# Optimization experiments

Measured on AMD Instinct MI355X. Metric: run time of the kernel, lower is better.

The kernel has to match this reference:

```python
import jax, jax.numpy as jnp
import numpy as np

N_NODES = 50000
N_EDGES = 400000


def _gcn_norm(edge_index, num_nodes):
    """Add self-loops and compute symmetric GCN normalization coefficients.

    Returns (src, dst, norm) where out[dst] += norm * h[src].
    """
    loop = jnp.arange(num_nodes, dtype=edge_index.dtype)
    src = jnp.concatenate([edge_index[0], loop])
    dst = jnp.concatenate([edge_index[1], loop])
    ones = jnp.ones(src.shape[0], dtype=jnp.float32)
    deg = jax.ops.segment_sum(ones, dst, num_segments=num_nodes)
    d_inv_sqrt = jnp.where(deg > 0, jax.lax.rsqrt(jnp.maximum(deg, 1.0)), 0.0)
    norm = d_inv_sqrt[src] * d_inv_sqrt[dst]
    return src, dst, norm


def _gcn_conv(x, W, b, src, dst, norm, num_nodes):
    h = x @ W                              # [N, out] dense GEMM first (PyG GCNConv order)
    msg = h[src] * norm[:, None]           # [E+N, out] gather + scale
    agg = jax.ops.segment_sum(msg, dst, num_segments=num_nodes)  # scatter-add
    return agg + b


def setup_inputs() -> dict:
    key = jax.random.key(0)
    k1, k2, k3, k4, k5, k6 = jax.random.split(key, 6)
    x = jax.random.normal(k1, (N_NODES, 128), dtype=jnp.float32)
    edge_index = jax.random.randint(k2, (2, N_EDGES), 0, N_NODES, dtype=jnp.int64)
    # Glorot-ish scaled params
    W1 = jax.random.normal(k3, (128, 512), dtype=jnp.float32) * (1.0 / np.sqrt(128))
    b1 = jnp.zeros((512,), dtype=jnp.float32)
    W2 = jax.random.normal(k4, (512, 250), dtype=jnp.float32) * (1.0 / np.sqrt(512))
    b2 = jnp.zeros((250,), dtype=jnp.float32)
    return {"x": x, "edge_index": edge_index, "W1": W1, "b1": b1, "W2": W2, "b2": b2}


def reference(x, edge_index, W1, b1, W2, b2):
    num_nodes = x.shape[0]
    src, dst, norm = _gcn_norm(edge_index, num_nodes)
    h = _gcn_conv(x, W1, b1, src, dst, norm, num_nodes)
    h = jax.nn.relu(h)
    h = _gcn_conv(h, W2, b2, src, dst, norm, num_nodes)
    return jax.nn.relu(h)
```

## Files before the change

### kernel.cpp

```cpp
#include <hip/hip_runtime.h>

constexpr int NN  = 50000;
constexpr int NE  = 400000;
constexpr int F0  = 128;
constexpr int F1  = 512;
constexpr int F2  = 250;
constexpr int MT  = 391;
constexpr int SCAN_N = 50176;
constexpr int SCAN_B = 49;

typedef short  short8 __attribute__((ext_vector_type(8)));
typedef float  f32x4  __attribute__((ext_vector_type(4)));

__device__ inline unsigned short f2bf(float f) {
    union { float f; unsigned u; } v; v.f = f;
    unsigned u = v.u;
    return (unsigned short)((u + 0x7FFFu + ((u >> 16) & 1u)) >> 16);
}
__device__ inline float bf2f(unsigned short h) {
    union { unsigned u; float f; } v; v.u = ((unsigned)h) << 16;
    return v.f;
}

__global__ void k_hist(const int4* __restrict__ dst4, int* __restrict__ cnt) {
    int t = blockIdx.x * 256 + threadIdx.x;
    if (t >= NE / 4) return;
    int4 d = dst4[t];
    atomicAdd(&cnt[d.x], 1); atomicAdd(&cnt[d.y], 1);
    atomicAdd(&cnt[d.z], 1); atomicAdd(&cnt[d.w], 1);
}

__global__ __launch_bounds__(256) void k_scanA(const int4* __restrict__ cnt4,
                                               int* __restrict__ bsum) {
    __shared__ int lds[256];
    const int b = blockIdx.x, t = threadIdx.x;
    int4 c = cnt4[b * 256 + t];
    lds[t] = c.x + c.y + c.z + c.w;
    __syncthreads();
    for (int d = 128; d > 0; d >>= 1) {
        if (t < d) lds[t] += lds[t + d];
        __syncthreads();
    }
    if (t == 0) bsum[b] = lds[0];
}
__global__ void k_scanB(const int* __restrict__ bsum, int* __restrict__ boff) {
    int t = threadIdx.x;
    int v = (t < SCAN_B) ? bsum[t] : 0;
    int orig = v;
    for (int d = 1; d < 64; d <<= 1) {
        int u = __shfl_up(v, d);
        if (t >= d) v += u;
    }
    if (t < SCAN_B) boff[t] = v - orig;
}
__global__ __launch_bounds__(256) void k_scanC(const int4* __restrict__ cnt4,
                                               const int* __restrict__ boff,
                                               int* __restrict__ off,
                                               float* __restrict__ dinv) {
    __shared__ int lds[256];
    const int b = blockIdx.x, t = threadIdx.x;
    int4 c = cnt4[b * 256 + t];
    int s = c.x + c.y + c.z + c.w;
    lds[t] = s;
    __syncthreads();
    for (int d = 1; d < 256; d <<= 1) {
        int add = (t >= d) ? lds[t - d] : 0;
        __syncthreads();
        lds[t] += add;
        __syncthreads();
    }
    int run = boff[b] + lds[t] - s;
    int base = b * 1024 + t * 4;
    if (base < NN) { off[base] = run; dinv[base] = rsqrtf((float)c.x + 1.0f); }
    run += c.x;
    if (base + 1 < NN) { off[base + 1] = run; dinv[base + 1] = rsqrtf((float)c.y + 1.0f); }
    run += c.y;
    if (base + 2 < NN) { off[base + 2] = run; dinv[base + 2] = rsqrtf((float)c.z + 1.0f); }
    run += c.z;
    if (base + 3 < NN) { off[base + 3] = run; dinv[base + 3] = rsqrtf((float)c.w + 1.0f); }
    if (b == 0 && t == 0) off[NN] = NE;
}

__global__ void k_bucket(const int4* __restrict__ src4, const int4* __restrict__ dst4,
                         const int* __restrict__ off, int* __restrict__ cnt,
                         int* __restrict__ csr) {
    int t = blockIdx.x * 256 + threadIdx.x;
    if (t >= NE / 4) return;
    int4 s = src4[t];
    int4 d = dst4[t];
    csr[off[d.x] + atomicSub(&cnt[d.x], 1) - 1] = s.x;
    csr[off[d.y] + atomicSub(&cnt[d.y], 1) - 1] = s.y;
    csr[off[d.z] + atomicSub(&cnt[d.z], 1) - 1] = s.z;
    csr[off[d.w] + atomicSub(&cnt[d.w], 1) - 1] = s.w;
}

__global__ __launch_bounds__(256) void k_prep(
        const float4* __restrict__ x4, const float* __restrict__ dinv,
        ushort4* __restrict__ xs,
        const float* __restrict__ W1, unsigned short* __restrict__ w1t,
        const float* __restrict__ W2, unsigned short* __restrict__ w2t) {
    int b = blockIdx.x;
    if (b < 6250) {
        int t = b * 256 + threadIdx.x;
        float dn = dinv[t >> 5];
        float4 v = x4[t];
        ushort4 o;
        o.x = f2bf(dn * v.x); o.y = f2bf(dn * v.y);
        o.z = f2bf(dn * v.z); o.w = f2bf(dn * v.w);
        xs[t] = o;
    } else if (b < 6250 + 256) {
        int t = (b - 6250) * 256 + threadIdx.x;
        int n = t >> 7, k = t & 127;
        w1t[t] = f2bf(W1[k * F1 + n]);
    } else {
        int t = (b - 6506) * 256 + threadIdx.x;
        int n = t >> 9, k = t & 511;
        w2t[t] = (n < F2) ? f2bf(W2[k * F2 + n]) : (unsigned short)0;
    }
}

__global__ __launch_bounds__(256) void k_gather1(
        const ushort4* __restrict__ xs, const int* __restrict__ off,
        const int* __restrict__ csr, const float* __restrict__ dinv,
        ushort4* __restrict__ agg) {
    int n = blockIdx.x * 8 + (threadIdx.x >> 5);
    int c = threadIdx.x & 31;
    if (n >= NN) return;
    float dn = dinv[n];
    ushort4 a = xs[(size_t)n * 32 + c];
    float sx = bf2f(a.x), sy = bf2f(a.y), sz = bf2f(a.z), sw = bf2f(a.w);
    int j = off[n], e1 = off[n + 1];
    for (; j + 4 <= e1; j += 4) {
        int s0 = csr[j], s1 = csr[j + 1], s2 = csr[j + 2], s3 = csr[j + 3];
        ushort4 v0 = xs[(size_t)s0 * 32 + c];
        ushort4 v1 = xs[(size_t)s1 * 32 + c];
        ushort4 v2 = xs[(size_t)s2 * 32 + c];
        ushort4 v3 = xs[(size_t)s3 * 32 + c];
        sx += bf2f(v0.x) + bf2f(v1.x) + bf2f(v2.x) + bf2f(v3.x);
        sy += bf2f(v0.y) + bf2f(v1.y) + bf2f(v2.y) + bf2f(v3.y);
        sz += bf2f(v0.z) + bf2f(v1.z) + bf2f(v2.z) + bf2f(v3.z);
        sw += bf2f(v0.w) + bf2f(v1.w) + bf2f(v2.w) + bf2f(v3.w);
    }
    for (; j < e1; ++j) {
        int s = csr[j];
        ushort4 v = xs[(size_t)s * 32 + c];
        sx += bf2f(v.x); sy += bf2f(v.y); sz += bf2f(v.z); sw += bf2f(v.w);
    }
    ushort4 o;
    o.x = f2bf(dn * sx); o.y = f2bf(dn * sy); o.z = f2bf(dn * sz); o.w = f2bf(dn * sw);
    agg[(size_t)n * 32 + c] = o;
}

__global__ __launch_bounds__(256) void k_gather2(
        const ushort4* __restrict__ t4, const int* __restrict__ off,
        const int* __restrict__ csr, const float* __restrict__ dinv,
        const float* __restrict__ b2, float* __restrict__ out) {
    int n = blockIdx.x * 4 + (threadIdx.x >> 6);
    int c = threadIdx.x & 63;
    if (n >= NN) return;
    float dn = dinv[n];
    ushort4 a = t4[(size_t)n * 64 + c];
    float sx = bf2f(a.x), sy = bf2f(a.y), sz = bf2f(a.z), sw = bf2f(a.w);
    int j = off[n], e1 = off[n + 1];
    for (; j + 4 <= e1; j += 4) {
        int s0 = csr[j], s1 = csr[j + 1], s2 = csr[j + 2], s3 = csr[j + 3];
        ushort4 v0 = t4[(size_t)s0 * 64 + c];
        ushort4 v1 = t4[(size_t)s1 * 64 + c];
        ushort4 v2 = t4[(size_t)s2 * 64 + c];
        ushort4 v3 = t4[(size_t)s3 * 64 + c];
        sx += bf2f(v0.x) + bf2f(v1.x) + bf2f(v2.x) + bf2f(v3.x);
        sy += bf2f(v0.y) + bf2f(v1.y) + bf2f(v2.y) + bf2f(v3.y);
        sz += bf2f(v0.z) + bf2f(v1.z) + bf2f(v2.z) + bf2f(v3.z);
        sw += bf2f(v0.w) + bf2f(v1.w) + bf2f(v2.w) + bf2f(v3.w);
    }
    for (; j < e1; ++j) {
        int s = csr[j];
        ushort4 v = t4[(size_t)s * 64 + c];
        sx += bf2f(v.x); sy += bf2f(v.y); sz += bf2f(v.z); sw += bf2f(v.w);
    }
    int f = c * 4;
    float* o = out + (size_t)n * F2;
    if (f     < F2) o[f]     = fmaxf(dn * sx + b2[f],     0.f);
    if (f + 1 < F2) o[f + 1] = fmaxf(dn * sy + b2[f + 1], 0.f);
    if (f + 2 < F2) o[f + 2] = fmaxf(dn * sz + b2[f + 2], 0.f);
    if (f + 3 < F2) o[f + 3] = fmaxf(dn * sw + b2[f + 3], 0.f);
}

__global__ __launch_bounds__(256) void k_gemm_bf16(
        const unsigned short* __restrict__ A, int lda,
        const unsigned short* __restrict__ Bt, int ldb,
        unsigned short* __restrict__ C, int ldc,
        const float* __restrict__ bias, int do_relu,
        const float* __restrict__ rowscale,
        int M, int K)
{
    __shared__ unsigned short As[128 * 32];
    __shared__ unsigned short Bs[128 * 32];

    const int tid = threadIdx.x;
    const int wv = tid >> 6, ln = tid & 63;
    const int m0 = blockIdx.y * 128, n0 = blockIdx.x * 128;
    const int wy = wv >> 1, wx = wv & 1;
    const int lane15 = ln & 15, quad = ln >> 4;

    const unsigned short* ag[2];
    const unsigned short* bg[2];
    int ldsoff[2];
#pragma unroll
    for (int i = 0; i < 2; ++i) {
        int c = (i * 4 + wv) * 64 + ln;
        int m = c >> 2, q = c & 3;
        int gq = q ^ ((m >> 1) & 3);
        int arow = m0 + m; if (arow > M - 1) arow = M - 1;
        ag[i] = A  + (size_t)arow * lda + gq * 8;
        bg[i] = Bt + (size_t)(n0 + m) * ldb + gq * 8;
        ldsoff[i] = (i * 4 + wv) * 512;
    }

    f32x4 acc[4][4];
#pragma unroll
    for (int fy = 0; fy < 4; ++fy)
#pragma unroll
        for (int fx = 0; fx < 4; ++fx)
            acc[fy][fx] = (f32x4)0.0f;

    for (int k0 = 0; k0 < K; k0 += 32) {
#pragma unroll
        for (int i = 0; i < 2; ++i) {
            __builtin_amdgcn_global_load_lds(
                (const __attribute__((address_space(1))) void*)ag[i],
                (__attribute__((address_space(3))) void*)(As + ldsoff[i]), 16, 0, 0);
            __builtin_amdgcn_global_load_lds(
                (const __attribute__((address_space(1))) void*)bg[i],
                (__attribute__((address_space(3))) void*)(Bs + ldsoff[i]), 16, 0, 0);
            ag[i] += 32; bg[i] += 32;
        }
        __syncthreads();

        short8 af[4], bf[4];
#pragma unroll
        for (int f = 0; f < 4; ++f) {
            int mA = wy * 64 + f * 16 + lane15;
            int sA = quad ^ ((mA >> 1) & 3);
            af[f] = *(const short8*)(As + mA * 32 + sA * 8);
            int nB = wx * 64 + f * 16 + lane15;
            int sB = quad ^ ((nB >> 1) & 3);
            bf[f] = *(const short8*)(Bs + nB * 32 + sB * 8);
        }
#pragma unroll
        for (int fy = 0; fy < 4; ++fy)
#pragma unroll
            for (int fx = 0; fx < 4; ++fx)
                acc[fy][fx] = __builtin_amdgcn_mfma_f32_16x16x32_bf16(
                    af[fy], bf[fx], acc[fy][fx], 0, 0, 0);
        __syncthreads();
    }

#pragma unroll
    for (int fy = 0; fy < 4; ++fy) {
        int rowb = m0 + wy * 64 + fy * 16 + quad * 4;
        float rs[4] = {1.f, 1.f, 1.f, 1.f};
        if (rowscale) {
#pragma unroll
            for (int r = 0; r < 4; ++r) {
                int row = rowb + r; if (row > M - 1) row = M - 1;
                rs[r] = rowscale[row];
            }
        }
#pragma unroll
        for (int fx = 0; fx < 4; ++fx) {
            int col = n0 + wx * 64 + fx * 16 + lane15;
            float bia = bias ? bias[col] : 0.0f;
            f32x4 v = acc[fy][fx];
#pragma unroll
            for (int r = 0; r < 4; ++r) {
                int row = rowb + r;
                if (row < M) {
                    float val = v[r] + bia;
                    if (do_relu) val = fmaxf(val, 0.0f);
                    val *= rs[r];
                    C[(size_t)row * ldc + col] = f2bf(val);
                }
            }
        }
    }
}

extern "C" void kernel_launch(void* const* d_in, const int* in_sizes, int n_in,
                              void* d_out, int out_size, void* d_ws, size_t ws_size,
                              hipStream_t stream) {
    const float* x  = (const float*)d_in[0];
    const int*   ei = (const int*)d_in[1];
    const float* W1 = (const float*)d_in[2];
    const float* b1 = (const float*)d_in[3];
    const float* W2 = (const float*)d_in[4];
    const float* b2 = (const float*)d_in[5];
    float* out = (float*)d_out;

    char* p = (char*)d_ws;
    auto carve = [&](size_t bytes) { char* r = p; p += (bytes + 255) & ~(size_t)255; return r; };
    float*          dinv = (float*)carve(NN * 4);
    int*            cnt  = (int*)carve(SCAN_N * 4);
    int*            off  = (int*)carve((NN + 1) * 4);
    int*            csr  = (int*)carve(NE * 4);
    int*            bsum = (int*)carve(64 * 4);
    int*            boff = (int*)carve(64 * 4);
    unsigned short* xs   = (unsigned short*)carve((size_t)NN * F0 * 2);
    unsigned short* agg1 = (unsigned short*)carve((size_t)NN * F0 * 2);
    unsigned short* h1   = (unsigned short*)carve((size_t)NN * F1 * 2);
    unsigned short* t2s  = (unsigned short*)carve((size_t)NN * 256 * 2);
    unsigned short* w1t  = (unsigned short*)carve((size_t)F1 * F0 * 2);
    unsigned short* w2t  = (unsigned short*)carve((size_t)256 * F1 * 2);

    hipMemsetAsync(cnt, 0, SCAN_N * sizeof(int), stream);
    k_hist <<<(NE / 4 + 255) / 256, 256, 0, stream>>>((const int4*)(ei + NE), cnt);
    k_scanA<<<SCAN_B, 256, 0, stream>>>((const int4*)cnt, bsum);
    k_scanB<<<1, 64, 0, stream>>>(bsum, boff);
    k_scanC<<<SCAN_B, 256, 0, stream>>>((const int4*)cnt, boff, off, dinv);
    k_bucket<<<(NE / 4 + 255) / 256, 256, 0, stream>>>(
        (const int4*)ei, (const int4*)(ei + NE), off, cnt, csr);

    k_prep<<<6250 + 256 + 512, 256, 0, stream>>>(
        (const float4*)x, dinv, (ushort4*)xs, W1, w1t, W2, w2t);

    k_gather1<<<(NN + 7) / 8, 256, 0, stream>>>((const ushort4*)xs, off, csr, dinv,
                                                (ushort4*)agg1);
    k_gemm_bf16<<<dim3(F1 / 128, MT), 256, 0, stream>>>(
        agg1, F0, w1t, F0, h1, F1, b1, 1, nullptr, NN, F0);

    k_gemm_bf16<<<dim3(256 / 128, MT), 256, 0, stream>>>(
        h1, F1, w2t, F1, t2s, 256, nullptr, 0, dinv, NN, F1);
    k_gather2<<<(NN + 3) / 4, 256, 0, stream>>>((const ushort4*)t2s, off, csr, dinv,
                                                b2, out);
}
```

Before: 292.1 us.

## Double-buffer LDS in bf16 GEMM and shrink M tile to 64 rows

The GEMM kernel now uses 64x128 output tiles instead of 128x128, which doubles the number of blocks launched for both layers. It also double-buffers the A and B shared-memory tiles, issuing the next K-slice's global-to-LDS loads before computing on the current slice, so one barrier per iteration replaces two. The intent is to raise occupancy and wave count on the GPU and to overlap global loads with MFMA work. The cost is less reuse of each B tile per block and more LDS per block.

```diff
diff --git a/kernel.cpp b/kernel.cpp
--- a/kernel.cpp
+++ b/kernel.cpp
@@ -5,7 +5,7 @@
 constexpr int F0  = 128;
 constexpr int F1  = 512;
 constexpr int F2  = 250;
-constexpr int MT  = 391;
+constexpr int MT64 = 782;
 constexpr int SCAN_N = 50176;
 constexpr int SCAN_B = 49;
 
@@ -194,71 +194,91 @@
         const float* __restrict__ rowscale,
         int M, int K)
 {
-    __shared__ unsigned short As[128 * 32];
-    __shared__ unsigned short Bs[128 * 32];
+    __shared__ unsigned short As[2][64 * 32];
+    __shared__ unsigned short Bs[2][128 * 32];
 
     const int tid = threadIdx.x;
     const int wv = tid >> 6, ln = tid & 63;
-    const int m0 = blockIdx.y * 128, n0 = blockIdx.x * 128;
+    const int m0 = blockIdx.y * 64, n0 = blockIdx.x * 128;
     const int wy = wv >> 1, wx = wv & 1;
     const int lane15 = ln & 15, quad = ln >> 4;
 
-    const unsigned short* ag[2];
-    const unsigned short* bg[2];
-    int ldsoff[2];
+    {
+    }
+    const int cA = tid, mA_ = cA >> 2, qA = cA & 3;
+    const int gqA = qA ^ ((mA_ >> 1) & 3);
+    int arow = m0 + mA_; if (arow > M - 1) arow = M - 1;
+    const unsigned short* agp = A + (size_t)arow * lda + gqA * 8;
+    const int aofs = wv * 512;
+
+    const unsigned short* bgp[2];
+    int bofs[2];
 #pragma unroll
     for (int i = 0; i < 2; ++i) {
         int c = (i * 4 + wv) * 64 + ln;
         int m = c >> 2, q = c & 3;
         int gq = q ^ ((m >> 1) & 3);
-        int arow = m0 + m; if (arow > M - 1) arow = M - 1;
-        ag[i] = A  + (size_t)arow * lda + gq * 8;
-        bg[i] = Bt + (size_t)(n0 + m) * ldb + gq * 8;
-        ldsoff[i] = (i * 4 + wv) * 512;
-    }
-
-    f32x4 acc[4][4];
-#pragma unroll
-    for (int fy = 0; fy < 4; ++fy)
+        bgp[i] = Bt + (size_t)(n0 + m) * ldb + gq * 8;
+        bofs[i] = (i * 4 + wv) * 512;
+    }
+
+    f32x4 acc[2][4];
+#pragma unroll
+    for (int fy = 0; fy < 2; ++fy)
 #pragma unroll
         for (int fx = 0; fx < 4; ++fx)
             acc[fy][fx] = (f32x4)0.0f;
 
-    for (int k0 = 0; k0 < K; k0 += 32) {
-#pragma unroll
-        for (int i = 0; i < 2; ++i) {
+    const int NK = K >> 5;
+
+    __builtin_amdgcn_global_load_lds(
+        (const __attribute__((address_space(1))) void*)agp,
+        (__attribute__((address_space(3))) void*)(&As[0][0] + aofs), 16, 0, 0);
+#pragma unroll
+    for (int i = 0; i < 2; ++i)
+        __builtin_amdgcn_global_load_lds(
+            (const __attribute__((address_space(1))) void*)bgp[i],
+            (__attribute__((address_space(3))) void*)(&Bs[0][0] + bofs[i]), 16, 0, 0);
+
+    for (int ks = 0; ks < NK; ++ks) {
+        __syncthreads();
+        if (ks + 1 < NK) {
+            int ko = (ks + 1) << 5;
+            int nb = (ks + 1) & 1;
             __builtin_amdgcn_global_load_lds(
-                (const __attribute__((address_space(1))) void*)ag[i],
-                (__attribute__((address_space(3))) void*)(As + ldsoff[i]), 16, 0, 0);
-            __builtin_amdgcn_global_load_lds(
-                (const __attribute__((address_space(1))) void*)bg[i],
-                (__attribute__((address_space(3))) void*)(Bs + ldsoff[i]), 16, 0, 0);
-            ag[i] += 32; bg[i] += 32;
-        }
-        __syncthreads();
-
-        short8 af[4], bf[4];
+                (const __attribute__((address_space(1))) void*)(agp + ko),
+                (__attribute__((address_space(3))) void*)(&As[nb][0] + aofs), 16, 0, 0);
+#pragma unroll
+            for (int i = 0; i < 2; ++i)
+                __builtin_amdgcn_global_load_lds(
+                    (const __attribute__((address_space(1))) void*)(bgp[i] + ko),
+                    (__attribute__((address_space(3))) void*)(&Bs[nb][0] + bofs[i]), 16, 0, 0);
+        }
+        const int b = ks & 1;
+        short8 af[2], bf[4];
+#pragma unroll
+        for (int f = 0; f < 2; ++f) {
+            int mA = wy * 32 + f * 16 + lane15;
+            int sA = quad ^ ((mA >> 1) & 3);
+            af[f] = *(const short8*)(&As[b][0] + mA * 32 + sA * 8);
+        }
 #pragma unroll
         for (int f = 0; f < 4; ++f) {
-            int mA = wy * 64 + f * 16 + lane15;
-            int sA = quad ^ ((mA >> 1) & 3);
-            af[f] = *(const short8*)(As + mA * 32 + sA * 8);
             int nB = wx * 64 + f * 16 + lane15;
             int sB = quad ^ ((nB >> 1) & 3);
-            bf[f] = *(const short8*)(Bs + nB * 32 + sB * 8);
-        }
-#pragma unroll
-        for (int fy = 0; fy < 4; ++fy)
+            bf[f] = *(const short8*)(&Bs[b][0] + nB * 32 + sB * 8);
+        }
+#pragma unroll
+        for (int fy = 0; fy < 2; ++fy)
 #pragma unroll
             for (int fx = 0; fx < 4; ++fx)
                 acc[fy][fx] = __builtin_amdgcn_mfma_f32_16x16x32_bf16(
                     af[fy], bf[fx], acc[fy][fx], 0, 0, 0);
-        __syncthreads();
-    }
-
-#pragma unroll
-    for (int fy = 0; fy < 4; ++fy) {
-        int rowb = m0 + wy * 64 + fy * 16 + quad * 4;
+    }
+
+#pragma unroll
+    for (int fy = 0; fy < 2; ++fy) {
+        int rowb = m0 + wy * 32 + fy * 16 + quad * 4;
         float rs[4] = {1.f, 1.f, 1.f, 1.f};
         if (rowscale) {
 #pragma unroll
@@ -325,10 +345,10 @@
 
     k_gather1<<<(NN + 7) / 8, 256, 0, stream>>>((const ushort4*)xs, off, csr, dinv,
                                                 (ushort4*)agg1);
-    k_gemm_bf16<<<dim3(F1 / 128, MT), 256, 0, stream>>>(
+    k_gemm_bf16<<<dim3(F1 / 128, MT64), 256, 0, stream>>>(
         agg1, F0, w1t, F0, h1, F1, b1, 1, nullptr, NN, F0);
 
-    k_gemm_bf16<<<dim3(256 / 128, MT), 256, 0, stream>>>(
+    k_gemm_bf16<<<dim3(256 / 128, MT64), 256, 0, stream>>>(
         h1, F1, w2t, F1, t2s, 256, nullptr, 0, dinv, NN, F1);
     k_gather2<<<(NN + 3) / 4, 256, 0, stream>>>((const ushort4*)t2s, off, csr, dinv,
                                                 b2, out);
```

Result: faster. 268.2 us (-8.2%).
